# Performance work log

Hardware: AMD Instinct MI355X
Metric: run time of the kernel (lower is better)

Reference implementation:

```python
import jax, jax.numpy as jnp
import numpy as np

B, T, H, C = 128, 1024, 512, 10


def setup_inputs() -> dict:
    key = jax.random.key(0)
    ks = jax.random.split(key, 8)
    s = 1.0 / np.sqrt(H)  # PyTorch LSTMCell/Linear default init scale
    return {
        "x": jax.random.normal(ks[0], (B, T), jnp.float32),
        "w_ih": jax.random.uniform(ks[1], (4 * H, 1), jnp.float32, -s, s),
        "w_hh": jax.random.uniform(ks[2], (4 * H, H), jnp.float32, -s, s),
        "b_ih": jax.random.uniform(ks[3], (4 * H,), jnp.float32, -s, s),
        "b_hh": jax.random.uniform(ks[4], (4 * H,), jnp.float32, -s, s),
        "w_t": jax.random.normal(ks[5], (2 * H, 1), jnp.float32) * 0.02,
        "w_fc": jax.random.uniform(ks[6], (C, H), jnp.float32, -s, s),
        "b_fc": jax.random.uniform(ks[7], (C,), jnp.float32, -s, s),
    }


def reference(x, w_ih, w_hh, b_ih, b_hh, w_t, w_fc, b_fc):
    # x: [B, T] scalar-per-step sequence (input_size == 1 in the original)
    Bz = x.shape[0]
    Hh = w_hh.shape[1]
    w1 = w_t[:Hh, 0]   # multiplies the new hidden h_t       [H]
    w2 = w_t[Hh:, 0]   # multiplies each history state h_j   [H]
    bias = b_ih + b_hh
    wih_row = w_ih[:, 0]  # [4H], since input_size == 1

    # Original computes, at step i, attn_c = sum_{j<=i} ((h_new@w1 + h_j@w2) * h_j)
    # over history [h_init=0, h_1, ..., h_i]. We keep running sums:
    #   S1 = sum_j h_j,   S2 = sum_j (h_j@w2) * h_j
    # so attn_c = (h_new@w1) * S1 + S2  -- identical math, O(T) instead of O(T^2).
    def step(carry, x_t):
        h, c, S1, S2 = carry
        gates = x_t[:, None] * wih_row[None, :] + h @ w_hh.T + bias  # [B,4H]
        i_g, f_g, g_g, o_g = jnp.split(gates, 4, axis=1)  # PyTorch gate order i,f,g,o
        c_new = jax.nn.sigmoid(f_g) * c + jax.nn.sigmoid(i_g) * jnp.tanh(g_g)
        h_new = jax.nn.sigmoid(o_g) * jnp.tanh(c_new)
        a = (h_new @ w1)[:, None]          # [B,1]
        attn = a * S1 + S2                 # [B,H]
        S1 = S1 + h_new
        S2 = S2 + (h_new @ w2)[:, None] * h_new
        return (h_new, c_new, S1, S2), (h_new, attn)

    z = jnp.zeros((Bz, Hh), x.dtype)
    _, (hs, attns) = jax.lax.scan(step, (z, z, z, z), x.T)  # [T,B,H] each
    out = jnp.transpose(hs + attns, (1, 0, 2))               # [B,T,H]
    return out @ w_fc.T + b_fc                               # [B,T,C]
```

## Files before the change

### kernel.cpp

```cpp
#include <hip/hip_runtime.h>
#include <math.h>

typedef __attribute__((ext_vector_type(8))) short bf16x8;
typedef __attribute__((ext_vector_type(4))) float f32x4;

static constexpr int Tt = 1024;
static constexpr int Hh = 512;
static constexpr int Cc = 10;

static constexpr int NXCD = 8;
static constexpr int BPX  = 32;
static constexpr int UPB  = 16;
static constexpr int NB   = 16;
static constexpr int THREADS = 256;
static constexpr int GRID = 256;

static constexpr size_t WS_HHI_B = 4096;
static constexpr size_t WS_HLO_B = 4096 + 32768;

__device__ __forceinline__ unsigned short f2bf(float f) {
    unsigned u = __builtin_bit_cast(unsigned, f);
    return (unsigned short)((u + 0x7FFFu + ((u >> 16) & 1u)) >> 16);
}
__device__ __forceinline__ float bf2f(unsigned short h) {
    unsigned u = ((unsigned)h) << 16;
    return __builtin_bit_cast(float, u);
}
__device__ __forceinline__ float dot4(float4 a, float4 b) {
    return a.x * b.x + a.y * b.y + a.z * b.z + a.w * b.w;
}

__global__ __launch_bounds__(THREADS, 1)
void lstm_fused(const float* __restrict__ x,
                const float* __restrict__ w_ih,
                const float* __restrict__ w_hh,
                const float* __restrict__ b_ih,
                const float* __restrict__ b_hh,
                const float* __restrict__ w_t,
                const float* __restrict__ w_fc,
                const float* __restrict__ b_fc,
                float* __restrict__ out,
                float* __restrict__ ws)
{
    const int tid  = threadIdx.x;
    const int lane = tid & 63;
    const int wv   = tid >> 6;

    int* bar      = (int*)ws;
    int* counters = (int*)ws + 256;
    unsigned short* hg_hi = (unsigned short*)((char*)ws + WS_HHI_B);
    unsigned short* hg_lo = (unsigned short*)((char*)ws + WS_HLO_B);

    __shared__ __align__(16) short wls_hi[64 * 512];
    __shared__ __align__(16) short wls_lo[64 * 512];
    __shared__ __align__(16) short hhi_ls[16 * 512];
    __shared__ __align__(16) short hlo_ls[16 * 512];
    float* gbuf = (float*)hhi_ls;
    int*   xchg = (int*)hlo_ls;

    if (tid == 0) {
        int xr;
        asm volatile("s_getreg_b32 %0, hwreg(20, 0, 32)" : "=s"(xr));
        const int xcd = xr & 7;
        xchg[0] = xcd;
        xchg[1] = atomicAdd(&counters[xcd * 32], 1) & 31;
    }
    __syncthreads();
    const int xcd  = xchg[0];
    const int rank = xchg[1];
    __syncthreads();
    int* mycnt = &bar[xcd * 32];

    {
        #pragma unroll
        for (int it = 0; it < 16; ++it) {
            const int idx = it * 256 + tid;
            const int lr = idx >> 6, kg = idx & 63;
            const int grow = (lr >> 4) * Hh + rank * UPB + (lr & 15);
            const float4* src = (const float4*)(w_hh + (size_t)grow * Hh + kg * 8);
            const float4 f0 = src[0], f1 = src[1];
            const float f[8] = { f0.x, f0.y, f0.z, f0.w, f1.x, f1.y, f1.z, f1.w };
            bf16x8 vhi, vlo;
            #pragma unroll
            for (int j = 0; j < 8; ++j) {
                const unsigned short h = f2bf(f[j]);
                vhi[j] = (short)h;
                vlo[j] = (short)f2bf(f[j] - bf2f(h));
            }
            const int off = (lr * 1024 + kg * 16) ^ ((lr & 7) << 4);
            *(bf16x8*)((char*)wls_hi + off) = vhi;
            *(bf16x8*)((char*)wls_lo + off) = vlo;
        }
    }

    const int u  = tid & 15;
    const int b_ = tid >> 4;
    const int gj = rank * UPB + u;
    const int gb = xcd * NB + b_;
    float wih_r[4], bias_r[4];
    #pragma unroll
    for (int g = 0; g < 4; ++g) {
        wih_r[g]  = w_ih[g * Hh + gj];
        bias_r[g] = b_ih[g * Hh + gj] + b_hh[g * Hh + gj];
    }
    float creg = 0.0f;

    const bool owner = (rank < NB);
    const int  gb_own = xcd * NB + rank;
    float S1w[Cc], S2w[Cc], bfc_r[Cc];
    #pragma unroll
    for (int c = 0; c < Cc; ++c) { S1w[c] = 0.f; S2w[c] = 0.f; bfc_r[c] = b_fc[c]; }

    const int arow  = wv * 16 + (lane & 15);
    const int aoff0 = arow * 1024 + ((lane >> 4) << 4);
    const int boff0 = (lane & 15) * 1024 + ((lane >> 4) << 4);
    const int xmask = (lane & 7) << 4;

    for (int t = 0; t < Tt; ++t) {
        const int rb = t & 1, wb = rb ^ 1;
        const float xv = x[(size_t)gb * Tt + t];

        if (t == 0) {
            const bf16x8 z = { 0, 0, 0, 0, 0, 0, 0, 0 };
            #pragma unroll
            for (int it = 0; it < 4; ++it) {
                const int idx = it * 256 + tid;
                const int row = idx >> 6, kg = idx & 63;
                const int off = (row * 1024 + kg * 16) ^ ((row & 7) << 4);
                *(bf16x8*)((char*)hhi_ls + off) = z;
                *(bf16x8*)((char*)hlo_ls + off) = z;
            }
        } else {
            const bf16x8* shi = (const bf16x8*)(hg_hi + (size_t)(rb * NXCD + xcd) * NB * Hh);
            const bf16x8* slo = (const bf16x8*)(hg_lo + (size_t)(rb * NXCD + xcd) * NB * Hh);
            #pragma unroll
            for (int it = 0; it < 4; ++it) {
                const int idx = it * 256 + tid;
                const int row = idx >> 6, kg = idx & 63;
                const bf16x8 vhi = shi[idx];
                const bf16x8 vlo = slo[idx];
                const int off = (row * 1024 + kg * 16) ^ ((row & 7) << 4);
                *(bf16x8*)((char*)hhi_ls + off) = vhi;
                *(bf16x8*)((char*)hlo_ls + off) = vlo;
            }
        }
        __syncthreads();

        f32x4 acc0 = { 0.f, 0.f, 0.f, 0.f };
        f32x4 acc1 = { 0.f, 0.f, 0.f, 0.f };
        f32x4 acc2 = { 0.f, 0.f, 0.f, 0.f };
        #pragma unroll
        for (int kk = 0; kk < 16; ++kk) {
            const int ao = (aoff0 + kk * 64) ^ xmask;
            const int bo = (boff0 + kk * 64) ^ xmask;
            const bf16x8 ahi = *(const bf16x8*)((const char*)wls_hi + ao);
            const bf16x8 alo = *(const bf16x8*)((const char*)wls_lo + ao);
            const bf16x8 bhi = *(const bf16x8*)((const char*)hhi_ls + bo);
            const bf16x8 blo = *(const bf16x8*)((const char*)hlo_ls + bo);
            acc0 = __builtin_amdgcn_mfma_f32_16x16x32_bf16(ahi, bhi, acc0, 0, 0, 0);
            acc1 = __builtin_amdgcn_mfma_f32_16x16x32_bf16(ahi, blo, acc1, 0, 0, 0);
            acc2 = __builtin_amdgcn_mfma_f32_16x16x32_bf16(alo, bhi, acc2, 0, 0, 0);
        }
        __syncthreads();

        {
            const int unit0 = (lane >> 4) * 4;
            const int batch = lane & 15;
            #pragma unroll
            for (int r = 0; r < 4; ++r)
                gbuf[(wv * 16 + unit0 + r) * 20 + batch] = acc0[r] + acc1[r] + acc2[r];
        }
        __syncthreads();

        {
            const float gi = gbuf[(0 * UPB + u) * 20 + b_] + xv * wih_r[0] + bias_r[0];
            const float gf = gbuf[(1 * UPB + u) * 20 + b_] + xv * wih_r[1] + bias_r[1];
            const float gg = gbuf[(2 * UPB + u) * 20 + b_] + xv * wih_r[2] + bias_r[2];
            const float go = gbuf[(3 * UPB + u) * 20 + b_] + xv * wih_r[3] + bias_r[3];
            const float si = 1.f / (1.f + expf(-gi));
            const float sf = 1.f / (1.f + expf(-gf));
            const float so = 1.f / (1.f + expf(-go));
            creg = sf * creg + si * tanhf(gg);
            const float hnew = so * tanhf(creg);
            const unsigned short hb = f2bf(hnew);
            const unsigned short lb = f2bf(hnew - bf2f(hb));
            const size_t hoff = ((size_t)(wb * NXCD + xcd) * NB + b_) * Hh + gj;
            hg_hi[hoff] = hb;
            hg_lo[hoff] = lb;
        }
        __syncthreads();

        if (tid == 0) {
            __hip_atomic_fetch_add(mycnt, 1, __ATOMIC_RELAXED,
                                   __HIP_MEMORY_SCOPE_AGENT);
            const int target = (t + 1) * BPX;
            int v = __hip_atomic_load(mycnt, __ATOMIC_RELAXED,
                                      __HIP_MEMORY_SCOPE_AGENT);
            while (v < target) {
                __builtin_amdgcn_s_sleep(2);
                v = __hip_atomic_load(mycnt, __ATOMIC_RELAXED,
                                      __HIP_MEMORY_SCOPE_AGENT);
            }
            asm volatile("buffer_inv\n\ts_waitcnt vmcnt(0)" ::: "memory");
        }
        __syncthreads();

        if (wv == 0 && owner) {
            const size_t rbase = ((size_t)(wb * NXCD + xcd) * NB + rank) * Hh + lane * 8;
            const bf16x8 vh = *(const bf16x8*)(hg_hi + rbase);
            const bf16x8 vl = *(const bf16x8*)(hg_lo + rbase);
            float f[8];
            #pragma unroll
            for (int j = 0; j < 8; ++j)
                f[j] = bf2f((unsigned short)vh[j]) + bf2f((unsigned short)vl[j]);
            const float4 hA = make_float4(f[0], f[1], f[2], f[3]);
            const float4 hB = make_float4(f[4], f[5], f[6], f[7]);
            const float4* wt4 = (const float4*)w_t;
            const float4* wf4 = (const float4*)w_fc;
            float r[12];
            r[0] = dot4(hA, wt4[lane * 2])       + dot4(hB, wt4[lane * 2 + 1]);
            r[1] = dot4(hA, wt4[128 + lane * 2]) + dot4(hB, wt4[128 + lane * 2 + 1]);
            #pragma unroll
            for (int c = 0; c < Cc; ++c)
                r[2 + c] = dot4(hA, wf4[c * 128 + lane * 2])
                         + dot4(hB, wf4[c * 128 + lane * 2 + 1]);
            #pragma unroll
            for (int m = 1; m <= 32; m <<= 1)
                #pragma unroll
                for (int k2 = 0; k2 < 12; ++k2)
                    r[k2] += __shfl_xor(r[k2], m, 64);

            if (lane == 0) {
                const float a = r[0], b2 = r[1];
                float* po = out + ((size_t)gb_own * Tt + t) * Cc;
                #pragma unroll
                for (int c = 0; c < Cc; ++c) {
                    const float hw = r[2 + c];
                    po[c] = hw + a * S1w[c] + S2w[c] + bfc_r[c];
                    S1w[c] += hw;
                    S2w[c] += b2 * hw;
                }
            }
        }
        __syncthreads();
    }
}

extern "C" void kernel_launch(void* const* d_in, const int* in_sizes, int n_in,
                              void* d_out, int out_size, void* d_ws, size_t ws_size,
                              hipStream_t stream)
{
    const float* xp  = (const float*)d_in[0];
    const float* wih = (const float*)d_in[1];
    const float* whh = (const float*)d_in[2];
    const float* bih = (const float*)d_in[3];
    const float* bhh = (const float*)d_in[4];
    const float* wt  = (const float*)d_in[5];
    const float* wfc = (const float*)d_in[6];
    const float* bfc = (const float*)d_in[7];
    float* outp = (float*)d_out;
    float* ws   = (float*)d_ws;

    (void)hipMemsetAsync(d_ws, 0, 4096, stream);

    hipLaunchKernelGGL(lstm_fused, dim3(GRID), dim3(THREADS), 0, stream,
                       xp, wih, whh, bih, bhh, wt, wfc, bfc, outp, ws);
}
```

Measured before the change: 4.774 ms.

## Replace atomic counter barrier with per-block flags, defer epilogue, fast activations

Replaces the per-XCD atomic counter barrier with per-block flag words that each block writes and 32 lanes poll together, which cuts atomic traffic and serialisation. The output projection for step t-1 is moved to the start of step t, so it overlaps the h load instead of adding its own barrier phase, with one extra loop iteration to drain the last step. Sigmoid and tanh now use the hardware exp2 and rcp intrinsics instead of expf and tanhf, which lowers precision slightly. The flag barrier depends on volatile stores and buffer_inv being visible in the right order across CUs.

Result: faster. 4.424 ms (-7.3%).

```diff
diff --git a/kernel.cpp b/kernel.cpp
--- a/kernel.cpp
+++ b/kernel.cpp
@@ -28,6 +28,14 @@
 }
 __device__ __forceinline__ float dot4(float4 a, float4 b) {
     return a.x * b.x + a.y * b.y + a.z * b.z + a.w * b.w;
+}
+__device__ __forceinline__ float fsig(float x) {
+    const float e = __builtin_amdgcn_exp2f(x * -1.44269504f);
+    return __builtin_amdgcn_rcpf(1.0f + e);
+}
+__device__ __forceinline__ float ftanh(float x) {
+    const float e = __builtin_amdgcn_exp2f(x * -2.88539008f);
+    return 2.0f * __builtin_amdgcn_rcpf(1.0f + e) - 1.0f;
 }
 
 __global__ __launch_bounds__(THREADS, 1)
@@ -46,7 +54,7 @@
     const int lane = tid & 63;
     const int wv   = tid >> 6;
 
-    int* bar      = (int*)ws;
+    int* flags    = (int*)ws;
     int* counters = (int*)ws + 256;
     unsigned short* hg_hi = (unsigned short*)((char*)ws + WS_HHI_B);
     unsigned short* hg_lo = (unsigned short*)((char*)ws + WS_HLO_B);
@@ -69,7 +77,7 @@
     const int xcd  = xchg[0];
     const int rank = xchg[1];
     __syncthreads();
-    int* mycnt = &bar[xcd * 32];
+    const int fbase = xcd * BPX;
 
     {
         #pragma unroll
@@ -116,9 +124,8 @@
     const int boff0 = (lane & 15) * 1024 + ((lane >> 4) << 4);
     const int xmask = (lane & 7) << 4;
 
-    for (int t = 0; t < Tt; ++t) {
+    for (int t = 0; t <= Tt; ++t) {
         const int rb = t & 1, wb = rb ^ 1;
-        const float xv = x[(size_t)gb * Tt + t];
 
         if (t == 0) {
             const bf16x8 z = { 0, 0, 0, 0, 0, 0, 0, 0 };
@@ -130,7 +137,7 @@
                 *(bf16x8*)((char*)hhi_ls + off) = z;
                 *(bf16x8*)((char*)hlo_ls + off) = z;
             }
-        } else {
+        } else if (t < Tt) {
             const bf16x8* shi = (const bf16x8*)(hg_hi + (size_t)(rb * NXCD + xcd) * NB * Hh);
             const bf16x8* slo = (const bf16x8*)(hg_lo + (size_t)(rb * NXCD + xcd) * NB * Hh);
             #pragma unroll
@@ -144,6 +151,47 @@
                 *(bf16x8*)((char*)hlo_ls + off) = vlo;
             }
         }
+
+        if (t > 0 && wv == 0 && owner) {
+            const size_t rbase = ((size_t)(rb * NXCD + xcd) * NB + rank) * Hh + lane * 8;
+            const bf16x8 vh = *(const bf16x8*)(hg_hi + rbase);
+            const bf16x8 vl = *(const bf16x8*)(hg_lo + rbase);
+            float f[8];
+            #pragma unroll
+            for (int j = 0; j < 8; ++j)
+                f[j] = bf2f((unsigned short)vh[j]) + bf2f((unsigned short)vl[j]);
+            const float4 hA = make_float4(f[0], f[1], f[2], f[3]);
+            const float4 hB = make_float4(f[4], f[5], f[6], f[7]);
+            const float4* wt4 = (const float4*)w_t;
+            const float4* wf4 = (const float4*)w_fc;
+            float r[12];
+            r[0] = dot4(hA, wt4[lane * 2])       + dot4(hB, wt4[lane * 2 + 1]);
+            r[1] = dot4(hA, wt4[128 + lane * 2]) + dot4(hB, wt4[128 + lane * 2 + 1]);
+            #pragma unroll
+            for (int c = 0; c < Cc; ++c)
+                r[2 + c] = dot4(hA, wf4[c * 128 + lane * 2])
+                         + dot4(hB, wf4[c * 128 + lane * 2 + 1]);
+            #pragma unroll
+            for (int m = 1; m <= 32; m <<= 1)
+                #pragma unroll
+                for (int k2 = 0; k2 < 12; ++k2)
+                    r[k2] += __shfl_xor(r[k2], m, 64);
+
+            if (lane == 0) {
+                const float a = r[0], b2 = r[1];
+                float* po = out + ((size_t)gb_own * Tt + (t - 1)) * Cc;
+                #pragma unroll
+                for (int c = 0; c < Cc; ++c) {
+                    const float hw = r[2 + c];
+                    po[c] = hw + a * S1w[c] + S2w[c] + bfc_r[c];
+                    S1w[c] += hw;
+                    S2w[c] += b2 * hw;
+                }
+            }
+        }
+        if (t == Tt) break;
+
+        const float xv = x[(size_t)gb * Tt + t];
         __syncthreads();
 
         f32x4 acc0 = { 0.f, 0.f, 0.f, 0.f };
@@ -177,11 +225,8 @@
             const float gf = gbuf[(1 * UPB + u) * 20 + b_] + xv * wih_r[1] + bias_r[1];
             const float gg = gbuf[(2 * UPB + u) * 20 + b_] + xv * wih_r[2] + bias_r[2];
             const float go = gbuf[(3 * UPB + u) * 20 + b_] + xv * wih_r[3] + bias_r[3];
-            const float si = 1.f / (1.f + expf(-gi));
-            const float sf = 1.f / (1.f + expf(-gf));
-            const float so = 1.f / (1.f + expf(-go));
-            creg = sf * creg + si * tanhf(gg);
-            const float hnew = so * tanhf(creg);
+            creg = fsig(gf) * creg + fsig(gi) * ftanh(gg);
+            const float hnew = fsig(go) * ftanh(creg);
             const unsigned short hb = f2bf(hnew);
             const unsigned short lb = f2bf(hnew - bf2f(hb));
             const size_t hoff = ((size_t)(wb * NXCD + xcd) * NB + b_) * Hh + gj;
@@ -190,57 +235,18 @@
         }
         __syncthreads();
 
-        if (tid == 0) {
-            __hip_atomic_fetch_add(mycnt, 1, __ATOMIC_RELAXED,
-                                   __HIP_MEMORY_SCOPE_AGENT);
-            const int target = (t + 1) * BPX;
-            int v = __hip_atomic_load(mycnt, __ATOMIC_RELAXED,
-                                      __HIP_MEMORY_SCOPE_AGENT);
-            while (v < target) {
-                __builtin_amdgcn_s_sleep(2);
-                v = __hip_atomic_load(mycnt, __ATOMIC_RELAXED,
-                                      __HIP_MEMORY_SCOPE_AGENT);
+        if (tid == 0)
+            *(volatile int*)(flags + fbase + rank) = t + 1;
+
+        if (tid < 32) {
+            const volatile int* fl = (const volatile int*)(flags + fbase + tid);
+            int v = *fl;
+            while (__any(v < t + 1)) {
+                __builtin_amdgcn_s_sleep(1);
+                asm volatile("buffer_inv\n\ts_waitcnt vmcnt(0)" ::: "memory");
+                v = *fl;
             }
             asm volatile("buffer_inv\n\ts_waitcnt vmcnt(0)" ::: "memory");
-        }
-        __syncthreads();
-
-        if (wv == 0 && owner) {
-            const size_t rbase = ((size_t)(wb * NXCD + xcd) * NB + rank) * Hh + lane * 8;
-            const bf16x8 vh = *(const bf16x8*)(hg_hi + rbase);
-            const bf16x8 vl = *(const bf16x8*)(hg_lo + rbase);
-            float f[8];
-            #pragma unroll
-            for (int j = 0; j < 8; ++j)
-                f[j] = bf2f((unsigned short)vh[j]) + bf2f((unsigned short)vl[j]);
-            const float4 hA = make_float4(f[0], f[1], f[2], f[3]);
-            const float4 hB = make_float4(f[4], f[5], f[6], f[7]);
-            const float4* wt4 = (const float4*)w_t;
-            const float4* wf4 = (const float4*)w_fc;
-            float r[12];
-            r[0] = dot4(hA, wt4[lane * 2])       + dot4(hB, wt4[lane * 2 + 1]);
-            r[1] = dot4(hA, wt4[128 + lane * 2]) + dot4(hB, wt4[128 + lane * 2 + 1]);
-            #pragma unroll
-            for (int c = 0; c < Cc; ++c)
-                r[2 + c] = dot4(hA, wf4[c * 128 + lane * 2])
-                         + dot4(hB, wf4[c * 128 + lane * 2 + 1]);
-            #pragma unroll
-            for (int m = 1; m <= 32; m <<= 1)
-                #pragma unroll
-                for (int k2 = 0; k2 < 12; ++k2)
-                    r[k2] += __shfl_xor(r[k2], m, 64);
-
-            if (lane == 0) {
-                const float a = r[0], b2 = r[1];
-                float* po = out + ((size_t)gb_own * Tt + t) * Cc;
-                #pragma unroll
-                for (int c = 0; c < Cc; ++c) {
-                    const float hw = r[2 + c];
-                    po[c] = hw + a * S1w[c] + S2w[c] + bfc_r[c];
-                    S1w[c] += hw;
-                    S2w[c] += b2 * hw;
-                }
-            }
         }
         __syncthreads();
     }
```
